# Optimization experiments

Hardware: AMD Instinct MI355X
Metric: run time of the kernel (lower is better)

The kernel has to match this reference:

```python
import jax, jax.numpy as jnp
import numpy as np

WEIGHTS = (1.428, 40.097)


def setup_inputs() -> dict:
    key = jax.random.key(0)
    k1, k2 = jax.random.split(key)
    N, C, H, W = 32, 2, 512, 512
    inputs = jax.random.uniform(k1, (N, C, H, W), dtype=jnp.float32)
    targets = jax.random.randint(k2, (N, H, W), 0, C, dtype=jnp.int32)
    return {"inputs": inputs, "targets": targets}


def reference(inputs, targets):
    # Lovasz hinge-style loss, vectorized over all N*C rows at once.
    N, C, H, W = inputs.shape
    P = H * W
    x = inputs.reshape(N, C, P)                                   # [N,C,P]
    # masks[n,c,p] = (targets[n,p] == c)
    masks = (targets.reshape(N, 1, P) == jnp.arange(C, dtype=targets.dtype).reshape(1, C, 1)).astype(x.dtype)

    distance = jnp.abs(masks - x)                                 # [N,C,P]
    order = jnp.argsort(-distance, axis=-1)                       # descending sort indices
    d_sorted = jnp.take_along_axis(distance, order, axis=-1)
    m_sorted = jnp.take_along_axis(masks, order, axis=-1)

    msum = jnp.sum(m_sorted, axis=-1, keepdims=True)              # [N,C,1]
    inter = msum - jnp.cumsum(m_sorted, axis=-1)
    union = msum + jnp.cumsum(1.0 - m_sorted, axis=-1)
    iou = 1.0 - inter / union                                     # [N,C,P]
    # gradient of Lovasz extension: first-difference of iou
    grad = jnp.concatenate([iou[..., :1], iou[..., 1:] - iou[..., :-1]], axis=-1)

    per_row = jnp.sum(d_sorted * grad, axis=-1)                   # [N,C]

    # rows skipped when mask empty AND no prediction > 0.25
    empty = (jnp.sum(masks, axis=-1) == 0) & (jnp.sum(x > 0.25, axis=-1) == 0)
    valid = jnp.logical_not(empty)                                # [N,C]

    w = jnp.asarray(WEIGHTS, dtype=x.dtype)                       # [C]
    total = jnp.sum(per_row * w[None, :] * valid.astype(x.dtype))
    non_empty = jnp.sum(valid.astype(x.dtype))
    return total / N / non_empty
```

## Files before the change

kernel.cpp:

```cpp
#include <hip/hip_runtime.h>

#define NN   32
#define CCH  2
#define PP   (512*512)
#define RR   (NN*CCH)
#define NB   256
#define CKS  32
#define CHUNK (PP/CKS)
#define HT   512
#define ST   256
#define COLS 32

static_assert(ST == NB, "scan assumes one bucket per thread");
static_assert(CHUNK == HT*16, "hist loop shape");
static_assert(RR <= 64, "final reduce assumes one wave");

__device__ __forceinline__ double iou_f(double msum, unsigned k, unsigned cs) {
    if (k == 0u) return 0.0;
    if (msum == 0.0) return 1.0;
    const double dk = (double)k, dcs = (double)cs;
    return 1.0 - (msum - dcs) / (msum + dk - dcs);
}

__global__ __launch_bounds__(HT, 4) void hist_kernel(
        const float* __restrict__ x, const int* __restrict__ tgt,
        unsigned* __restrict__ g_part, unsigned* __restrict__ g_pos,
        unsigned* __restrict__ g_ticket)
{
    __shared__ unsigned s_h[CCH*NB*COLS];
    __shared__ unsigned s_posr[HT/64][2];

    const int nb  = blockIdx.x;
    const int n   = nb / CKS, ck = nb % CKS;
    const int tid = threadIdx.x;
    const int col = tid & 31;

    if (nb == 0 && tid == 0) *g_ticket = 0u;

    #pragma unroll
    for (int i = 0; i < CCH*NB*COLS/HT; ++i) s_h[i*HT + tid] = 0u;
    __syncthreads();

    const float* x0 = x   + ((size_t)(n*CCH + 0))*PP + (size_t)ck*CHUNK;
    const float* x1 = x   + ((size_t)(n*CCH + 1))*PP + (size_t)ck*CHUNK;
    const int*   tr = tgt + (size_t)n*PP            + (size_t)ck*CHUNK;

    const int p0 = tid*8, p1 = HT*8 + tid*8;
    const float4 A0 = *reinterpret_cast<const float4*>(x0 + p0);
    const float4 A1 = *reinterpret_cast<const float4*>(x0 + p0 + 4);
    const float4 B0 = *reinterpret_cast<const float4*>(x1 + p0);
    const float4 B1 = *reinterpret_cast<const float4*>(x1 + p0 + 4);
    const int4   T0 = *reinterpret_cast<const int4*>(tr + p0);
    const int4   T1 = *reinterpret_cast<const int4*>(tr + p0 + 4);
    const float4 C0 = *reinterpret_cast<const float4*>(x0 + p1);
    const float4 C1 = *reinterpret_cast<const float4*>(x0 + p1 + 4);
    const float4 D0 = *reinterpret_cast<const float4*>(x1 + p1);
    const float4 D1 = *reinterpret_cast<const float4*>(x1 + p1 + 4);
    const int4   U0 = *reinterpret_cast<const int4*>(tr + p1);
    const int4   U1 = *reinterpret_cast<const int4*>(tr + p1 + 4);

    unsigned pos0 = 0, pos1 = 0;
    auto proc = [&](const float4& a0, const float4& a1,
                    const float4& b0, const float4& b1,
                    const int4& t0, const int4& t1) {
        const float xs0[8] = {a0.x,a0.y,a0.z,a0.w, a1.x,a1.y,a1.z,a1.w};
        const float xs1[8] = {b0.x,b0.y,b0.z,b0.w, b1.x,b1.y,b1.z,b1.w};
        const int   ts [8] = {t0.x,t0.y,t0.z,t0.w, t1.x,t1.y,t1.z,t1.w};
        #pragma unroll
        for (int j = 0; j < 8; ++j) {
            const bool z = (ts[j] == 0);
            const float d0 = z ? (1.0f - xs0[j]) : xs0[j];
            const float d1 = z ? xs1[j] : (1.0f - xs1[j]);
            int k0 = (int)(d0 * (float)NB); k0 = k0 > NB-1 ? NB-1 : k0;
            int k1 = (int)(d1 * (float)NB); k1 = k1 > NB-1 ? NB-1 : k1;
            atomicAdd(&s_h[(0*NB + k0)*COLS + col], 0x10000u | (z ? 1u : 0u));
            atomicAdd(&s_h[(1*NB + k1)*COLS + col], 0x10000u | (z ? 0u : 1u));
            pos0 += (xs0[j] > 0.25f) ? 1u : 0u;
            pos1 += (xs1[j] > 0.25f) ? 1u : 0u;
        }
    };
    proc(A0, A1, B0, B1, T0, T1);
    proc(C0, C1, D0, D1, U0, U1);

    for (int off = 32; off; off >>= 1) {
        pos0 += __shfl_down(pos0, off);
        pos1 += __shfl_down(pos1, off);
    }
    if ((tid & 63) == 0) { s_posr[tid>>6][0] = pos0; s_posr[tid>>6][1] = pos1; }
    __syncthreads();

    if (tid == 0) {
        unsigned q0 = 0, q1 = 0;
        #pragma unroll
        for (int w = 0; w < HT/64; ++w) { q0 += s_posr[w][0]; q1 += s_posr[w][1]; }
        g_pos[nb*CCH + 0] = q0; g_pos[nb*CCH + 1] = q1;
    }

    {
        const unsigned base = tid * COLS;
        unsigned sum = 0;
        #pragma unroll
        for (int c = 0; c < COLS; ++c) sum += s_h[base + ((c + tid) & 31)];
        g_part[(size_t)nb * (CCH*NB) + tid] = sum;
    }
}

__global__ __launch_bounds__(ST) void scan_kernel(
        const unsigned* __restrict__ g_part, const unsigned* __restrict__ g_pos,
        float* __restrict__ g_row, float* __restrict__ g_valid,
        unsigned* __restrict__ g_ticket, float* __restrict__ out)
{
    __shared__ unsigned long long s_wsum[ST/64];
    __shared__ double   s_red[ST/64];
    __shared__ unsigned s_flag;

    const int r = blockIdx.x;
    const int n = r / CCH, c = r % CCH;
    const int tid = threadIdx.x, lane = tid & 63, wv = tid >> 6;

    const int bk = NB-1 - tid;
    unsigned lc = 0, lo = 0;
    #pragma unroll
    for (int b = 0; b < CKS; ++b) {
        const unsigned v = g_part[(size_t)(n*CKS + b)*(CCH*NB) + c*NB + bk];
        lc += v >> 16; lo += v & 0xffffu;
    }

    const unsigned long long v =
        ((unsigned long long)lc << 32) | (unsigned long long)lo;
    unsigned long long s = v;
    #pragma unroll
    for (int off = 1; off < 64; off <<= 1) {
        const unsigned long long t = __shfl_up(s, off, 64);
        if (lane >= off) s += t;
    }
    if (lane == 63) s_wsum[wv] = s;
    __syncthreads();
    unsigned long long woff = 0, tot = 0;
    #pragma unroll
    for (int w = 0; w < ST/64; ++w) {
        const unsigned long long u = s_wsum[w];
        tot += u;
        if (w < wv) woff += u;
    }
    const unsigned long long excl = s + woff - v;
    const unsigned msum = (unsigned)(tot & 0xffffffffu);
    const unsigned k  = (unsigned)(excl >> 32);
    const unsigned cs = (unsigned)(excl & 0xffffffffu);

    double acc = 0.0;
    if (lc) {
        const double dmsum = (double)msum;
        const double ip  = iou_f(dmsum, k, cs);
        const double in_ = iou_f(dmsum, k + lc, cs + lo);
        acc = (((double)bk + 0.5) * (1.0/(double)NB)) * (in_ - ip);
    }
    for (int off = 32; off; off >>= 1) acc += __shfl_down(acc, off);
    if (lane == 0) s_red[wv] = acc;
    __syncthreads();
    if (tid == 0) {
        double t = 0.0;
        #pragma unroll
        for (int w = 0; w < ST/64; ++w) t += s_red[w];
        unsigned pos = 0;
        for (int b = 0; b < CKS; ++b) pos += g_pos[(n*CKS + b)*CCH + c];
        const bool valid = !(msum == 0u && pos == 0u);
        const double W[CCH] = {1.428, 40.097};
        g_row[r]   = valid ? (float)(t * W[c]) : 0.f;
        g_valid[r] = valid ? 1.f : 0.f;
        __threadfence();
        s_flag = atomicAdd(g_ticket, 1u);
    }
    __syncthreads();

    if (s_flag == RR - 1) {
        __threadfence();
        if (tid < 64) {
            const volatile float* vr = g_row;
            const volatile float* vv = g_valid;
            double t  = (tid < RR) ? (double)vr[tid] : 0.0;
            double vl = (tid < RR) ? (double)vv[tid] : 0.0;
            for (int off = 32; off; off >>= 1) {
                t  += __shfl_down(t, off);
                vl += __shfl_down(vl, off);
            }
            if (tid == 0) out[0] = (float)(t / (double)NN / vl);
        }
    }
}

extern "C" void kernel_launch(void* const* d_in, const int* in_sizes, int n_in,
                              void* d_out, int out_size, void* d_ws, size_t ws_size,
                              hipStream_t stream) {
    const float* x   = (const float*)d_in[0];
    const int*   tgt = (const int*)d_in[1];
    float* out = (float*)d_out;

    const size_t SZP = (size_t)NN * CKS * CCH * NB;
    unsigned* g_part  = (unsigned*)d_ws;
    unsigned* g_pos   = g_part + SZP;
    float*    g_row   = (float*)(g_pos + NN*CKS*CCH);
    float*    g_valid = g_row + RR;
    unsigned* g_ticket = (unsigned*)(g_valid + RR);

    hist_kernel<<<NN*CKS, HT, 0, stream>>>(x, tgt, g_part, g_pos, g_ticket);
    scan_kernel<<<RR, ST, 0, stream>>>(g_part, g_pos, g_row, g_valid, g_ticket, out);
}
```

Baseline: 29.77 us.

## Halve histogram grid, drop replicated LDS histograms, software-prefetch four granules

```diff
diff --git a/kernel.cpp b/kernel.cpp
--- a/kernel.cpp
+++ b/kernel.cpp
@@ -5,14 +5,18 @@
 #define PP   (512*512)
 #define RR   (NN*CCH)
 #define NB   256
-#define CKS  32
-#define CHUNK (PP/CKS)
+#define BPI  16
+#define GRID (NN*BPI)
+#define SPAN (PP/BPI)
 #define HT   512
+#define GRAN (HT*8)
+#define NG   (SPAN/GRAN)
 #define ST   256
-#define COLS 32
 
 static_assert(ST == NB, "scan assumes one bucket per thread");
-static_assert(CHUNK == HT*16, "hist loop shape");
+static_assert(HT == 2*NB, "partial writeout shape");
+static_assert(NG == 4, "manual prefetch unroll below assumes 4 granules");
+static_assert(SPAN < 65536, "packed 16-bit cnt would overflow");
 static_assert(RR <= 64, "final reduce assumes one wave");
 
 __device__ __forceinline__ double iou_f(double msum, unsigned k, unsigned cs) {
@@ -22,50 +26,51 @@
     return 1.0 - (msum - dcs) / (msum + dk - dcs);
 }
 
+struct Batch {
+    float4 a0, a1;
+    float4 b0, b1;
+    int4   t0, t1;
+};
+
 __global__ __launch_bounds__(HT, 4) void hist_kernel(
         const float* __restrict__ x, const int* __restrict__ tgt,
         unsigned* __restrict__ g_part, unsigned* __restrict__ g_pos,
         unsigned* __restrict__ g_ticket)
 {
-    __shared__ unsigned s_h[CCH*NB*COLS];
+    __shared__ unsigned s_h0[NB];
+    __shared__ unsigned s_h1[NB];
     __shared__ unsigned s_posr[HT/64][2];
 
     const int nb  = blockIdx.x;
-    const int n   = nb / CKS, ck = nb % CKS;
+    const int n   = nb / BPI, blk = nb % BPI;
     const int tid = threadIdx.x;
-    const int col = tid & 31;
 
     if (nb == 0 && tid == 0) *g_ticket = 0u;
 
-    #pragma unroll
-    for (int i = 0; i < CCH*NB*COLS/HT; ++i) s_h[i*HT + tid] = 0u;
-    __syncthreads();
-
-    const float* x0 = x   + ((size_t)(n*CCH + 0))*PP + (size_t)ck*CHUNK;
-    const float* x1 = x   + ((size_t)(n*CCH + 1))*PP + (size_t)ck*CHUNK;
-    const int*   tr = tgt + (size_t)n*PP            + (size_t)ck*CHUNK;
-
-    const int p0 = tid*8, p1 = HT*8 + tid*8;
-    const float4 A0 = *reinterpret_cast<const float4*>(x0 + p0);
-    const float4 A1 = *reinterpret_cast<const float4*>(x0 + p0 + 4);
-    const float4 B0 = *reinterpret_cast<const float4*>(x1 + p0);
-    const float4 B1 = *reinterpret_cast<const float4*>(x1 + p0 + 4);
-    const int4   T0 = *reinterpret_cast<const int4*>(tr + p0);
-    const int4   T1 = *reinterpret_cast<const int4*>(tr + p0 + 4);
-    const float4 C0 = *reinterpret_cast<const float4*>(x0 + p1);
-    const float4 C1 = *reinterpret_cast<const float4*>(x0 + p1 + 4);
-    const float4 D0 = *reinterpret_cast<const float4*>(x1 + p1);
-    const float4 D1 = *reinterpret_cast<const float4*>(x1 + p1 + 4);
-    const int4   U0 = *reinterpret_cast<const int4*>(tr + p1);
-    const int4   U1 = *reinterpret_cast<const int4*>(tr + p1 + 4);
+    if (tid < NB) s_h0[tid] = 0u; else s_h1[tid - NB] = 0u;
+    __syncthreads();
+
+    const float* x0 = x   + ((size_t)(n*CCH + 0))*PP + (size_t)blk*SPAN;
+    const float* x1 = x   + ((size_t)(n*CCH + 1))*PP + (size_t)blk*SPAN;
+    const int*   tr = tgt + (size_t)n*PP            + (size_t)blk*SPAN;
 
     unsigned pos0 = 0, pos1 = 0;
-    auto proc = [&](const float4& a0, const float4& a1,
-                    const float4& b0, const float4& b1,
-                    const int4& t0, const int4& t1) {
-        const float xs0[8] = {a0.x,a0.y,a0.z,a0.w, a1.x,a1.y,a1.z,a1.w};
-        const float xs1[8] = {b0.x,b0.y,b0.z,b0.w, b1.x,b1.y,b1.z,b1.w};
-        const int   ts [8] = {t0.x,t0.y,t0.z,t0.w, t1.x,t1.y,t1.z,t1.w};
+
+    auto load = [&](int g) -> Batch {
+        Batch b;
+        const int p = g*GRAN + tid*8;
+        b.a0 = *reinterpret_cast<const float4*>(x0 + p);
+        b.a1 = *reinterpret_cast<const float4*>(x0 + p + 4);
+        b.b0 = *reinterpret_cast<const float4*>(x1 + p);
+        b.b1 = *reinterpret_cast<const float4*>(x1 + p + 4);
+        b.t0 = *reinterpret_cast<const int4*>(tr + p);
+        b.t1 = *reinterpret_cast<const int4*>(tr + p + 4);
+        return b;
+    };
+    auto proc = [&](const Batch& b) {
+        const float xs0[8] = {b.a0.x,b.a0.y,b.a0.z,b.a0.w, b.a1.x,b.a1.y,b.a1.z,b.a1.w};
+        const float xs1[8] = {b.b0.x,b.b0.y,b.b0.z,b.b0.w, b.b1.x,b.b1.y,b.b1.z,b.b1.w};
+        const int   ts [8] = {b.t0.x,b.t0.y,b.t0.z,b.t0.w, b.t1.x,b.t1.y,b.t1.z,b.t1.w};
         #pragma unroll
         for (int j = 0; j < 8; ++j) {
             const bool z = (ts[j] == 0);
@@ -73,14 +78,21 @@
             const float d1 = z ? xs1[j] : (1.0f - xs1[j]);
             int k0 = (int)(d0 * (float)NB); k0 = k0 > NB-1 ? NB-1 : k0;
             int k1 = (int)(d1 * (float)NB); k1 = k1 > NB-1 ? NB-1 : k1;
-            atomicAdd(&s_h[(0*NB + k0)*COLS + col], 0x10000u | (z ? 1u : 0u));
-            atomicAdd(&s_h[(1*NB + k1)*COLS + col], 0x10000u | (z ? 0u : 1u));
+            atomicAdd(&s_h0[k0], 0x10000u | (z ? 1u : 0u));
+            atomicAdd(&s_h1[k1], 0x10000u | (z ? 0u : 1u));
             pos0 += (xs0[j] > 0.25f) ? 1u : 0u;
             pos1 += (xs1[j] > 0.25f) ? 1u : 0u;
         }
     };
-    proc(A0, A1, B0, B1, T0, T1);
-    proc(C0, C1, D0, D1, U0, U1);
+
+    Batch c0 = load(0);
+    Batch c1 = load(1);
+    proc(c0);
+    Batch c2 = load(2);
+    proc(c1);
+    Batch c3 = load(3);
+    proc(c2);
+    proc(c3);
 
     for (int off = 32; off; off >>= 1) {
         pos0 += __shfl_down(pos0, off);
@@ -95,14 +107,7 @@
         for (int w = 0; w < HT/64; ++w) { q0 += s_posr[w][0]; q1 += s_posr[w][1]; }
         g_pos[nb*CCH + 0] = q0; g_pos[nb*CCH + 1] = q1;
     }
-
-    {
-        const unsigned base = tid * COLS;
-        unsigned sum = 0;
-        #pragma unroll
-        for (int c = 0; c < COLS; ++c) sum += s_h[base + ((c + tid) & 31)];
-        g_part[(size_t)nb * (CCH*NB) + tid] = sum;
-    }
+    g_part[(size_t)nb*(CCH*NB) + tid] = (tid < NB) ? s_h0[tid] : s_h1[tid - NB];
 }
 
 __global__ __launch_bounds__(ST) void scan_kernel(
@@ -121,8 +126,8 @@
     const int bk = NB-1 - tid;
     unsigned lc = 0, lo = 0;
     #pragma unroll
-    for (int b = 0; b < CKS; ++b) {
-        const unsigned v = g_part[(size_t)(n*CKS + b)*(CCH*NB) + c*NB + bk];
+    for (int b = 0; b < BPI; ++b) {
+        const unsigned v = g_part[(size_t)(n*BPI + b)*(CCH*NB) + c*NB + bk];
         lc += v >> 16; lo += v & 0xffffu;
     }
 
@@ -163,7 +168,7 @@
         #pragma unroll
         for (int w = 0; w < ST/64; ++w) t += s_red[w];
         unsigned pos = 0;
-        for (int b = 0; b < CKS; ++b) pos += g_pos[(n*CKS + b)*CCH + c];
+        for (int b = 0; b < BPI; ++b) pos += g_pos[(n*BPI + b)*CCH + c];
         const bool valid = !(msum == 0u && pos == 0u);
         const double W[CCH] = {1.428, 40.097};
         g_row[r]   = valid ? (float)(t * W[c]) : 0.f;
@@ -196,13 +201,13 @@
     const int*   tgt = (const int*)d_in[1];
     float* out = (float*)d_out;
 
-    const size_t SZP = (size_t)NN * CKS * CCH * NB;
+    const size_t SZP = (size_t)GRID * CCH * NB;
     unsigned* g_part  = (unsigned*)d_ws;
     unsigned* g_pos   = g_part + SZP;
-    float*    g_row   = (float*)(g_pos + NN*CKS*CCH);
+    float*    g_row   = (float*)(g_pos + GRID*CCH);
     float*    g_valid = g_row + RR;
     unsigned* g_ticket = (unsigned*)(g_valid + RR);
 
-    hist_kernel<<<NN*CKS, HT, 0, stream>>>(x, tgt, g_part, g_pos, g_ticket);
+    hist_kernel<<<GRID, HT, 0, stream>>>(x, tgt, g_part, g_pos, g_ticket);
     scan_kernel<<<RR, ST, 0, stream>>>(g_part, g_pos, g_row, g_valid, g_ticket, out);
 }
```

Result: faster. 27.77 us (median of 2 runs) (-6.7%).
